# Optimization experiments

Measured on AMD Instinct MI355X. Metric: run time of the kernel, lower is better.

Reference implementation:

```python
import jax, jax.numpy as jnp
import numpy as np

B, T, D, HS = 8, 2048, 768, 64
H = D // HS  # 12 heads
LN_EPS = 1e-5


def setup_inputs() -> dict:
    key = jax.random.key(0)
    ks = jax.random.split(key, 8)
    s = 0.02
    x = jax.random.normal(ks[0], (B, T, D), jnp.float32)
    Wx = jax.random.normal(ks[1], (D, D), jnp.float32) * s
    Ww = jax.random.normal(ks[2], (D, D), jnp.float32) * 0.01  # w_proj.weight ~ N(0,0.01)
    # w_proj bias schedule: logit(1 - linspace(0.9,0.999,H)) per head, expanded over head_size
    r_sched = jnp.linspace(0.9, 0.999, H)
    w_target = 1.0 - r_sched
    bw = jnp.log(w_target / (1.0 - w_target))          # logit
    bw = jnp.repeat(bw[:, None], HS, axis=1).reshape(-1)  # (D,)
    Wk = jax.random.normal(ks[3], (D, D), jnp.float32) * s
    Wv = jax.random.normal(ks[4], (D, D), jnp.float32) * s
    Wr = jax.random.normal(ks[5], (D, D), jnp.float32) * s
    Wo = jax.random.normal(ks[6], (D, D), jnp.float32) * s
    gamma = jnp.ones((D,), jnp.float32)
    beta = jnp.zeros((D,), jnp.float32)
    return {"x": x, "Wx": Wx, "Ww": Ww, "bw": bw, "Wk": Wk, "Wv": Wv,
            "Wr": Wr, "Wo": Wo, "gamma": gamma, "beta": beta}


def _layernorm(x, gamma, beta):
    mu = jnp.mean(x, axis=-1, keepdims=True)
    var = jnp.mean(jnp.square(x - mu), axis=-1, keepdims=True)
    return (x - mu) * jax.lax.rsqrt(var + LN_EPS) * gamma + beta


def _selective_scan(k, v, w):
    """k,v,w: (T,B,H,HS). State S: (B,H,HS,HS).
    S_t = (1 - w_t) * S_{t-1} (decay along key dim) + k_t (x) v_t;  y_t = k_t . S_t."""
    S0 = jnp.zeros((B, H, HS, HS), k.dtype)

    def step(S, inp):
        kt, vt, wt = inp  # each (B,H,HS)
        S = S * (1.0 - wt)[..., :, None] + kt[..., :, None] * vt[..., None, :]
        yt = jnp.einsum('bhi,bhij->bhj', kt, S)
        return S, yt

    _, ys = jax.lax.scan(step, S0, (k, v, w))
    return ys  # (T,B,H,HS)


def reference(x, Wx, Ww, bw, Wk, Wv, Wr, Wo, gamma, beta):
    xn = _layernorm(x, gamma, beta)                       # (B,T,D)
    xp = jnp.einsum('btd,ed->bte', xn, Wx)                # x_proj
    w = jax.nn.sigmoid(jnp.einsum('bte,fe->btf', xp, Ww) + bw)
    k = jnp.einsum('btd,ed->bte', xn, Wk)
    v = jnp.einsum('btd,ed->bte', xn, Wv)
    r = jax.nn.sigmoid(jnp.einsum('btd,ed->bte', xn, Wr))

    def to_scan(a):  # (B,T,D) -> (T,B,H,HS)
        return a.reshape(B, T, H, HS).transpose(1, 0, 2, 3)

    ys = _selective_scan(to_scan(k), to_scan(v), to_scan(w))  # (T,B,H,HS)
    y = ys.transpose(1, 0, 2, 3).reshape(B, T, D)
    y = y * r
    return jnp.einsum('btd,ed->bte', y, Wo)
```

## Files before the change

### kernel.cpp

```cpp
#include <hip/hip_runtime.h>

#define B_ 8
#define T_ 2048
#define D_ 768
#define H_ 12
#define HS_ 64
#define LN_EPS 1e-5f
#define NC 32
#define TC 64

typedef __attribute__((ext_vector_type(8))) short bf16x8;
typedef __attribute__((ext_vector_type(4))) float f32x4;

__device__ __forceinline__ ushort f2bf(float f) {
  unsigned u = __builtin_bit_cast(unsigned, f);
  unsigned r = (u + 0x7FFFu + ((u >> 16) & 1u)) >> 16;
  return (ushort)r;
}
__device__ __forceinline__ float bf2f(ushort u) {
  return __builtin_bit_cast(float, ((unsigned)u) << 16);
}

__device__ __forceinline__ int fragaddr(int t, int i) {
  return ((t >> 4) * 2 + (i >> 5)) * 512 + ((((i >> 3) & 3) * 16) + (t & 15)) * 8 + (i & 7);
}
__device__ __forceinline__ int fragswz(int i) {
  return (((i >> 3) & 3) << 3) ^ (((i >> 5) & 1) << 5);
}

__global__ __launch_bounds__(256) void zero_out_kernel(float* __restrict__ out, int n) {
  for (int i = blockIdx.x * 256 + threadIdx.x; i < n; i += gridDim.x * 256)
    out[i] = 0.f;
}

__global__ __launch_bounds__(256) void prepln_kernel(
    const float* __restrict__ x, const float* __restrict__ gamma,
    const float* __restrict__ beta, ushort* __restrict__ xn,
    const float* __restrict__ w0, const float* __restrict__ w1,
    const float* __restrict__ w2, const float* __restrict__ w3,
    const float* __restrict__ w4, const float* __restrict__ Wx,
    ushort* __restrict__ dst, ushort* __restrict__ WxT) {
  __shared__ ushort tile[32][33];
  const int bid = blockIdx.x;
  if (bid < 4096) {
    const int wv = threadIdx.x >> 6;
    const int lane = threadIdx.x & 63;
    const int row = bid * 4 + wv;
    const float* xr = x + (size_t)row * D_;
    float4 a[3];
#pragma unroll
    for (int s = 0; s < 3; ++s)
      a[s] = *reinterpret_cast<const float4*>(xr + s * 256 + lane * 4);
    float sum = 0.f;
#pragma unroll
    for (int s = 0; s < 3; ++s) sum += a[s].x + a[s].y + a[s].z + a[s].w;
#pragma unroll
    for (int off = 32; off; off >>= 1) sum += __shfl_xor(sum, off);
    float mu = sum * (1.f / 768.f);
    float vs = 0.f;
#pragma unroll
    for (int s = 0; s < 3; ++s) {
      float dx = a[s].x - mu, dy = a[s].y - mu, dz = a[s].z - mu, dw = a[s].w - mu;
      vs += dx * dx + dy * dy + dz * dz + dw * dw;
    }
#pragma unroll
    for (int off = 32; off; off >>= 1) vs += __shfl_xor(vs, off);
    float rs = rsqrtf(vs * (1.f / 768.f) + LN_EPS);
    ushort* orow = xn + (size_t)row * D_;
#pragma unroll
    for (int s = 0; s < 3; ++s) {
      int col = s * 256 + lane * 4;
      float4 g = *reinterpret_cast<const float4*>(gamma + col);
      float4 bb = *reinterpret_cast<const float4*>(beta + col);
      ushort4 o;
      o.x = f2bf((a[s].x - mu) * rs * g.x + bb.x);
      o.y = f2bf((a[s].y - mu) * rs * g.y + bb.y);
      o.z = f2bf((a[s].z - mu) * rs * g.z + bb.z);
      o.w = f2bf((a[s].w - mu) * rs * g.w + bb.w);
      *reinterpret_cast<ushort4*>(orow + col) = o;
    }
  } else if (bid < 4672) {
    const float* srcs[5] = {w0, w1, w2, w3, w4};
    const int slots[5] = {0, 1, 2, 4, 5};
    int idx = ((bid - 4096) * 256 + threadIdx.x) * 4;
#pragma unroll
    for (int s = 0; s < 5; ++s) {
      float4 v = *reinterpret_cast<const float4*>(srcs[s] + idx);
      ushort4 o;
      o.x = f2bf(v.x); o.y = f2bf(v.y); o.z = f2bf(v.z); o.w = f2bf(v.w);
      *reinterpret_cast<ushort4*>(dst + (size_t)slots[s] * 589824 + idx) = o;
    }
  } else {
    const int q = bid - 4672;
    const int bx = (q % 24) * 32;
    const int by = (q / 24) * 32;
    const int tx = threadIdx.x & 31, ty = threadIdx.x >> 5;
#pragma unroll
    for (int r = 0; r < 32; r += 8)
      tile[ty + r][tx] = f2bf(Wx[(size_t)(by + ty + r) * 768 + bx + tx]);
    __syncthreads();
#pragma unroll
    for (int r = 0; r < 32; r += 8)
      WxT[(size_t)(bx + ty + r) * 768 + by + tx] = tile[tx][ty + r];
  }
}

__global__ __launch_bounds__(512, 4) void gemm_p(
    const ushort* __restrict__ A, const ushort* __restrict__ W,
    float* __restrict__ Cf,
    ushort* __restrict__ d0, ushort* __restrict__ d1,
    ushort* __restrict__ d2, ushort* __restrict__ d3, int mode) {
  __shared__ __align__(16) ushort lds[36864];
  const int tid = threadIdx.x;
  const int wid = tid >> 6;
  const int lane = tid & 63;
  const int wr = wid >> 2, wc = wid & 3;
  const int fr = lane & 15, fq = lane >> 4;
  const int m0 = blockIdx.x * 128, n0 = blockIdx.y * 256;
  const int strow = tid >> 2;
  const int stseg = (tid & 3) ^ ((strow >> 1) & 3);
  const int rseg = fq ^ ((fr >> 1) & 3);

  f32x4 acc[4][4];
#pragma unroll
  for (int m = 0; m < 4; ++m)
#pragma unroll
    for (int n = 0; n < 4; ++n) acc[m][n] = (f32x4){0.f, 0.f, 0.f, 0.f};

#define STAGE_T(kk0, b)                                                           \
  {                                                                               \
    const ushort* sa_ = A + (size_t)(m0 + strow) * 768 + (kk0) + stseg * 8;       \
    __builtin_amdgcn_global_load_lds(                                             \
        (const __attribute__((address_space(1))) void*)sa_,                       \
        (__attribute__((address_space(3))) void*)(lds + (b) * 4096 + tid * 8),    \
        16, 0, 0);                                                                \
    _Pragma("unroll") for (int j = 0; j < 2; ++j) {                               \
      const ushort* sb_ =                                                         \
          W + (size_t)(n0 + j * 128 + strow) * 768 + (kk0) + stseg * 8;           \
      __builtin_amdgcn_global_load_lds(                                           \
          (const __attribute__((address_space(1))) void*)sb_,                     \
          (__attribute__((address_space(3))) void*)(lds + 12288 + (b) * 8192 +    \
                                                    j * 4096 + tid * 8),          \
          16, 0, 0);                                                              \
    }                                                                             \
  }

  STAGE_T(0, 0);
  STAGE_T(32, 1);
  STAGE_T(64, 2);
  asm volatile("s_waitcnt vmcnt(6)" ::: "memory");
  __builtin_amdgcn_s_barrier();

#pragma unroll 3
  for (int t = 0; t < 24; ++t) {
    const int buf = t % 3;
    bf16x8 aF[4], bF[4];
#pragma unroll
    for (int mi = 0; mi < 4; ++mi)
      aF[mi] = *reinterpret_cast<const bf16x8*>(
          lds + buf * 4096 + (wr * 64 + mi * 16 + fr) * 32 + rseg * 8);
#pragma unroll
    for (int nf = 0; nf < 4; ++nf)
      bF[nf] = *reinterpret_cast<const bf16x8*>(
          lds + 12288 + buf * 8192 + (wc * 64 + nf * 16 + fr) * 32 + rseg * 8);
    __builtin_amdgcn_s_setprio(1);
#pragma unroll
    for (int mi = 0; mi < 4; ++mi)
#pragma unroll
      for (int nf = 0; nf < 4; ++nf)
        acc[mi][nf] = __builtin_amdgcn_mfma_f32_16x16x32_bf16(
            aF[mi], bF[nf], acc[mi][nf], 0, 0, 0);
    __builtin_amdgcn_s_setprio(0);
    __builtin_amdgcn_s_barrier();
    if (t + 3 < 24) {
      STAGE_T((t + 3) * 32, buf);
      asm volatile("s_waitcnt vmcnt(6)" ::: "memory");
    } else if (t == 21) {
      asm volatile("s_waitcnt vmcnt(3)" ::: "memory");
    } else if (t == 22) {
      asm volatile("s_waitcnt vmcnt(0)" ::: "memory");
    }
    __builtin_amdgcn_s_barrier();
  }
#undef STAGE_T

  const int r0 = fq * 4;
  if (mode == 5) {
    const int sel = n0 >= 2304 ? 3 : n0 >= 1536 ? 2 : n0 >= 768 ? 1 : 0;
    const int nb = n0 - sel * 768;
    if (sel == 1) {
#pragma unroll
      for (int mf = 0; mf < 4; ++mf)
#pragma unroll
        for (int nf = 0; nf < 4; ++nf) {
          int gr = m0 + wr * 64 + mf * 16 + r0;
          int gc = nb + wc * 64 + nf * 16 + fr;
          int b = gr >> 11, t = gr & 2047;
          int c = t >> 6, s0 = t & 63;
          int h = gc >> 6, j = gc & 63;
          size_t addr = ((size_t)((b * 12 + h) * 32 + c)) * 4096 +
                        (size_t)(((j >> 4) * 2 + (s0 >> 5)) * 512 +
                                 (((s0 >> 3) & 3) * 16 + (j & 15)) * 8 + (s0 & 7));
          ushort4 o;
          o.x = f2bf(acc[mf][nf][0]); o.y = f2bf(acc[mf][nf][1]);
          o.z = f2bf(acc[mf][nf][2]); o.w = f2bf(acc[mf][nf][3]);
          *reinterpret_cast<ushort4*>(d1 + addr) = o;
        }
    } else if (sel == 2) {
#pragma unroll
      for (int mf = 0; mf < 4; ++mf)
#pragma unroll
        for (int nf = 0; nf < 4; ++nf) {
          int gr = m0 + wr * 64 + mf * 16 + r0;
          int gc = nb + wc * 64 + nf * 16 + fr;
          int b = gr >> 11, t = gr & 2047;
          int c = t >> 6, tin = t & 63;
          int h = gc >> 6, j = gc & 63;
          size_t addr = ((size_t)((b * 12 + h) * 32 + c)) * 4096 +
                        (size_t)(((tin >> 4) * 64 + ((tin >> 2) & 3) * 16 + (j & 15)) * 16 +
                                 (j >> 4) * 4);
          ushort4 o;
          o.x = f2bf(1.f / (1.f + __expf(-acc[mf][nf][0])));
          o.y = f2bf(1.f / (1.f + __expf(-acc[mf][nf][1])));
          o.z = f2bf(1.f / (1.f + __expf(-acc[mf][nf][2])));
          o.w = f2bf(1.f / (1.f + __expf(-acc[mf][nf][3])));
          *reinterpret_cast<ushort4*>(d2 + addr) = o;
        }
    } else {
      ushort* dst = sel == 0 ? d0 : d3;
#pragma unroll
      for (int mf = 0; mf < 4; ++mf)
#pragma unroll
        for (int nf = 0; nf < 4; ++nf) {
          int gr = m0 + wr * 64 + mf * 16 + r0;
          int gc = nb + wc * 64 + nf * 16 + fr;
#pragma unroll
          for (int rr = 0; rr < 4; ++rr)
            dst[(size_t)(gr + rr) * 768 + gc] = f2bf(acc[mf][nf][rr]);
        }
    }
  } else {
#pragma unroll
    for (int mf = 0; mf < 4; ++mf)
#pragma unroll
      for (int nf = 0; nf < 4; ++nf) {
        int gr = m0 + wr * 64 + mf * 16 + r0;
        int gc = n0 + wc * 64 + nf * 16 + fr;
#pragma unroll
        for (int rr = 0; rr < 4; ++rr)
          Cf[(size_t)(gr + rr) * 768 + gc] = acc[mf][nf][rr];
      }
  }
}

__global__ __launch_bounds__(256) void scan_mc3(
    const ushort* __restrict__ kb, const ushort* __restrict__ zb,
    const ushort* __restrict__ vbF, const float* __restrict__ bwp,
    ushort* __restrict__ McT, float* __restrict__ aend) {
  __shared__ ushort kt[64 * 72];
  __shared__ ushort zt[64 * 72];
  __shared__ ushort kIAfA[4096];
  __shared__ float part[256];
  const int bh = blockIdx.x, c = blockIdx.y;
  const int b = bh / H_, h = bh % H_;
  const int tid = threadIdx.x;
  const int w = tid >> 6, lane = tid & 63;
  const int fr = lane & 15, fq = lane >> 4;
  const int row = tid >> 2, c16 = (tid & 3) * 16;
  const float bwh = bwp[h * 64];

  {
    const ushort* gk = kb + ((size_t)(b * T_ + c * TC + row)) * 768 + h * 64 + c16;
    const ushort* gz = zb + ((size_t)(b * T_ + c * TC + row)) * 768 + h * 64 + c16;
    uint4 k0 = *(const uint4*)gk, k1 = *(const uint4*)(gk + 8);
    uint4 z0 = *(const uint4*)gz, z1 = *(const uint4*)(gz + 8);
    *reinterpret_cast<uint4*>(&kt[row * 72 + c16]) = k0;
    *reinterpret_cast<uint4*>(&kt[row * 72 + c16 + 8]) = k1;
    *reinterpret_cast<uint4*>(&zt[row * 72 + c16]) = z0;
    *reinterpret_cast<uint4*>(&zt[row * 72 + c16 + 8]) = z1;
  }
  bf16x8 vfr[8];
  {
    const ushort* vch = vbF + ((size_t)bh * NC + c) * 4096;
#pragma unroll
    for (int f = 0; f < 8; ++f)
      vfr[f] = *reinterpret_cast<const bf16x8*>(vch + f * 512 + lane * 8);
  }
  __syncthreads();
  float dreg[16];
  float p = 1.f;
#pragma unroll
  for (int tt = 0; tt < 16; ++tt) {
    float z = bf2f(zt[(w * 16 + tt) * 72 + lane]);
    float d = 1.f / (1.f + __expf(z + bwh));
    dreg[tt] = d;
    p *= d;
  }
  part[w * 64 + lane] = p;
  __syncthreads();
  float a = 1.f;
  for (int w2 = 0; w2 < w; ++w2) a *= part[w2 * 64 + lane];
  if (w == 0)
    aend[((size_t)bh * NC + c) * 64 + lane] =
        part[lane] * part[64 + lane] * part[128 + lane] * part[192 + lane];
#pragma unroll
  for (int tt = 0; tt < 16; ++tt) {
    int t = w * 16 + tt;
    float k = bf2f(kt[t * 72 + lane]);
    a *= dreg[tt];
    kIAfA[fragaddr(lane, t)] = f2bf(k / a);
  }
  __syncthreads();

  bf16x8 af2[2];
#pragma unroll
  for (int kk = 0; kk < 2; ++kk)
    af2[kk] = *reinterpret_cast<const bf16x8*>(&kIAfA[(w * 2 + kk) * 512 + lane * 8]);
  f32x4 accM[4];
#pragma unroll
  for (int nf = 0; nf < 4; ++nf) accM[nf] = (f32x4){0.f, 0.f, 0.f, 0.f};
#pragma unroll
  for (int kk = 0; kk < 2; ++kk)
#pragma unroll
    for (int nf = 0; nf < 4; ++nf)
      accM[nf] = __builtin_amdgcn_mfma_f32_16x16x32_bf16(af2[kk], vfr[nf * 2 + kk], accM[nf], 0, 0, 0);
  ushort* mch = McT + ((size_t)bh * NC + c) * 4096;
#pragma unroll
  for (int nf = 0; nf < 4; ++nf) {
    ushort4 o;
    o.x = f2bf(accM[nf][0]); o.y = f2bf(accM[nf][1]);
    o.z = f2bf(accM[nf][2]); o.w = f2bf(accM[nf][3]);
    *reinterpret_cast<ushort4*>(&mch[(nf * 16 + fr) * 64 + w * 16 + fq * 4]) = o;
  }
}

__global__ __launch_bounds__(256) void scan_chain3(
    const ushort* __restrict__ McT, const float* __restrict__ aend,
    ushort* __restrict__ S0F) {
  const int bh = blockIdx.x;
  const int j = threadIdx.x >> 2;
  const int i0 = blockIdx.y * 32 + (threadIdx.x & 3) * 8;
  const int fbase = ((j >> 4) * 2 + (i0 >> 5)) * 512 + (((i0 >> 3) & 3) * 16 + (j & 15)) * 8;
  const ushort* mbase = McT + ((size_t)bh * NC) * 4096 + j * 64 + i0;
  const float* abase = aend + ((size_t)bh * NC) * 64 + i0;
  float S[8];
#pragma unroll
  for (int p = 0; p < 8; ++p) S[p] = 0.f;

  ushort4 m0 = *reinterpret_cast<const ushort4*>(mbase);
  ushort4 m1 = *reinterpret_cast<const ushort4*>(mbase + 4);
  float4 a0 = *(const float4*)(abase);
  float4 a1 = *(const float4*)(abase + 4);
  ushort4 n0 = *reinterpret_cast<const ushort4*>(mbase + 4096);
  ushort4 n1 = *reinterpret_cast<const ushort4*>(mbase + 4096 + 4);
  float4 b0 = *(const float4*)(abase + 64);
  float4 b1 = *(const float4*)(abase + 64 + 4);

  for (int c = 0; c < NC; ++c) {
    int cn2 = c + 2 < NC ? c + 2 : NC - 1;
    ushort4 p0 = *reinterpret_cast<const ushort4*>(mbase + (size_t)cn2 * 4096);
    ushort4 p1 = *reinterpret_cast<const ushort4*>(mbase + (size_t)cn2 * 4096 + 4);
    float4 q0 = *(const float4*)(abase + (size_t)cn2 * 64);
    float4 q1 = *(const float4*)(abase + (size_t)cn2 * 64 + 4);

    ushort* s0 = S0F + ((size_t)bh * NC + c) * 4096 + fbase;
    ushort4 o0, o1;
    o0.x = f2bf(S[0]); o0.y = f2bf(S[1]); o0.z = f2bf(S[2]); o0.w = f2bf(S[3]);
    o1.x = f2bf(S[4]); o1.y = f2bf(S[5]); o1.z = f2bf(S[6]); o1.w = f2bf(S[7]);
    *reinterpret_cast<ushort4*>(s0) = o0;
    *reinterpret_cast<ushort4*>(s0 + 4) = o1;

    S[0] = a0.x * (S[0] + bf2f(m0.x));
    S[1] = a0.y * (S[1] + bf2f(m0.y));
    S[2] = a0.z * (S[2] + bf2f(m0.z));
    S[3] = a0.w * (S[3] + bf2f(m0.w));
    S[4] = a1.x * (S[4] + bf2f(m1.x));
    S[5] = a1.y * (S[5] + bf2f(m1.y));
    S[6] = a1.z * (S[6] + bf2f(m1.z));
    S[7] = a1.w * (S[7] + bf2f(m1.w));

    m0 = n0; m1 = n1; a0 = b0; a1 = b1;
    n0 = p0; n1 = p1; b0 = q0; b1 = q1;
  }
}

__global__ __launch_bounds__(256, 2) void scan_y3(
    const ushort* __restrict__ kb, const ushort* __restrict__ zb,
    const ushort* __restrict__ vbF, const ushort* __restrict__ rbF,
    const ushort* __restrict__ S0F, const float* __restrict__ bwp,
    ushort* __restrict__ yrow) {
  __shared__ ushort kt[64 * 72];
  __shared__ ushort zt[64 * 72];
  __shared__ ushort kAf[4096];
  __shared__ ushort kIAfB[4096];
  __shared__ ushort Am[64 * 72];
  __shared__ float part[256];
  const int bh = blockIdx.x, c = blockIdx.y;
  const int b = bh / H_, h = bh % H_;
  const int tid = threadIdx.x;
  const int w = tid >> 6, lane = tid & 63;
  const int fr = lane & 15, fq = lane >> 4;
  const int row = tid >> 2, c16 = (tid & 3) * 16;
  const float bwh = bwp[h * 64];
  const int swz = fragswz(lane);

  {
    const ushort* gk = kb + ((size_t)(b * T_ + c * TC + row)) * 768 + h * 64 + c16;
    const ushort* gz = zb + ((size_t)(b * T_ + c * TC + row)) * 768 + h * 64 + c16;
    uint4 k0 = *(const uint4*)gk, k1 = *(const uint4*)(gk + 8);
    uint4 z0 = *(const uint4*)gz, z1 = *(const uint4*)(gz + 8);
    *reinterpret_cast<uint4*>(&kt[row * 72 + c16]) = k0;
    *reinterpret_cast<uint4*>(&kt[row * 72 + c16 + 8]) = k1;
    *reinterpret_cast<uint4*>(&zt[row * 72 + c16]) = z0;
    *reinterpret_cast<uint4*>(&zt[row * 72 + c16 + 8]) = z1;
  }
  bf16x8 vfr[8], s0fr[8];
  {
    const ushort* vch = vbF + ((size_t)bh * NC + c) * 4096;
    const ushort* s0ch = S0F + ((size_t)bh * NC + c) * 4096;
#pragma unroll
    for (int f = 0; f < 8; ++f) {
      vfr[f] = *reinterpret_cast<const bf16x8*>(vch + f * 512 + lane * 8);
      s0fr[f] = *reinterpret_cast<const bf16x8*>(s0ch + f * 512 + lane * 8);
    }
  }
  ushort4 rp0, rp1, rp2, rp3;
  {
    const ushort* rch = rbF + ((size_t)bh * NC + c) * 4096 + tid * 16;
    rp0 = *reinterpret_cast<const ushort4*>(rch);
    rp1 = *reinterpret_cast<const ushort4*>(rch + 4);
    rp2 = *reinterpret_cast<const ushort4*>(rch + 8);
    rp3 = *reinterpret_cast<const ushort4*>(rch + 12);
  }
  const ushort rl[16] = {rp0.x, rp0.y, rp0.z, rp0.w, rp1.x, rp1.y, rp1.z, rp1.w,
                         rp2.x, rp2.y, rp2.z, rp2.w, rp3.x, rp3.y, rp3.z, rp3.w};
  __syncthreads();
  float dreg[16];
  float p = 1.f;
#pragma unroll
  for (int tt = 0; tt < 16; ++tt) {
    float z = bf2f(zt[(w * 16 + tt) * 72 + lane]);
    float d = 1.f / (1.f + __expf(z + bwh));
    dreg[tt] = d;
    p *= d;
  }
  part[w * 64 + lane] = p;
  __syncthreads();
  float a = 1.f;
  for (int w2 = 0; w2 < w; ++w2) a *= part[w2 * 64 + lane];
#pragma unroll
  for (int tt = 0; tt < 16; ++tt) {
    int t = w * 16 + tt;
    float k = bf2f(kt[t * 72 + lane]);
    a *= dreg[tt];
    int ad = fragaddr(t, lane) ^ swz;
    kAf[ad] = f2bf(k * a);
    kIAfB[ad] = f2bf(k / a);
  }
  __syncthreads();

  bf16x8 af[2];
#pragma unroll
  for (int kk = 0; kk < 2; ++kk) {
    int ra = ((w * 2 + kk) * 512 + lane * 8) ^ (((lane >> 4) << 3) ^ (kk << 5));
    af[kk] = *reinterpret_cast<const bf16x8*>(&kAf[ra]);
  }
  {
    f32x4 accA[4];
#pragma unroll
    for (int nf = 0; nf < 4; ++nf) accA[nf] = (f32x4){0.f, 0.f, 0.f, 0.f};
#pragma unroll
    for (int kk = 0; kk < 2; ++kk)
#pragma unroll
      for (int nf = 0; nf < 4; ++nf) {
        int rb8 = ((nf * 2 + kk) * 512 + lane * 8) ^ (((lane >> 4) << 3) ^ (kk << 5));
        bf16x8 b8 = *reinterpret_cast<const bf16x8*>(&kIAfB[rb8]);
        accA[nf] = __builtin_amdgcn_mfma_f32_16x16x32_bf16(af[kk], b8, accA[nf], 0, 0, 0);
      }
#pragma unroll
    for (int nf = 0; nf < 4; ++nf)
#pragma unroll
      for (int q = 0; q < 4; ++q) {
        int t = w * 16 + fq * 4 + q;
        int s = nf * 16 + fr;
        Am[t * 72 + s] = f2bf((s <= t) ? accA[nf][q] : 0.f);
      }
  }
  __syncthreads();

  f32x4 accY[4];
#pragma unroll
  for (int nf = 0; nf < 4; ++nf) accY[nf] = (f32x4){0.f, 0.f, 0.f, 0.f};
#pragma unroll
  for (int kk = 0; kk < 2; ++kk)
#pragma unroll
    for (int nf = 0; nf < 4; ++nf)
      accY[nf] = __builtin_amdgcn_mfma_f32_16x16x32_bf16(af[kk], s0fr[nf * 2 + kk], accY[nf], 0, 0, 0);
#pragma unroll
  for (int kk = 0; kk < 2; ++kk) {
    bf16x8 am8 = *reinterpret_cast<const bf16x8*>(&Am[(w * 16 + fr) * 72 + kk * 32 + fq * 8]);
#pragma unroll
    for (int nf = 0; nf < 4; ++nf)
      accY[nf] = __builtin_amdgcn_mfma_f32_16x16x32_bf16(am8, vfr[nf * 2 + kk], accY[nf], 0, 0, 0);
  }
#pragma unroll
  for (int nf = 0; nf < 4; ++nf)
#pragma unroll
    for (int q = 0; q < 4; ++q) {
      int t = w * 16 + fq * 4 + q;
      int j = nf * 16 + fr;
      size_t go = ((size_t)(b * T_ + c * TC + t)) * 768 + h * 64 + j;
      yrow[go] = f2bf(accY[nf][q] * bf2f(rl[nf * 4 + q]));
    }
}

extern "C" void kernel_launch(void* const* d_in, const int* in_sizes, int n_in,
                              void* d_out, int out_size, void* d_ws, size_t ws_size,
                              hipStream_t stream) {
  const float* x     = (const float*)d_in[0];
  const float* Wx    = (const float*)d_in[1];
  const float* Ww    = (const float*)d_in[2];
  const float* bw    = (const float*)d_in[3];
  const float* Wk    = (const float*)d_in[4];
  const float* Wv    = (const float*)d_in[5];
  const float* Wr    = (const float*)d_in[6];
  const float* Wo    = (const float*)d_in[7];
  const float* gamma = (const float*)d_in[8];
  const float* beta  = (const float*)d_in[9];
  float* out = (float*)d_out;

  const size_t NEED = 208404480ull;
  if (ws_size < NEED) {
    zero_out_kernel<<<2048, 256, 0, stream>>>(out, out_size);
    return;
  }

  char* ws = (char*)d_ws;
  ushort* xn  = (ushort*)ws;
  ushort* wb  = (ushort*)(ws + 25165824);
  ushort* WxT = (ushort*)(ws + 32243712);
  ushort* kb  = (ushort*)(ws + 57409536);
  ushort* vbF = (ushort*)(ws + 82575360);
  ushort* rbF = (ushort*)(ws + 107741184);
  ushort* yr  = (ushort*)(ws + 132907008);
  ushort* zb  = (ushort*)(ws + 158072832);
  ushort* McT = (ushort*)ws;
  ushort* S0F = (ushort*)(ws + 32243712);
  float*  aendb = (float*)(ws + 132907008);

  ushort* WcatB = wb;
  ushort* Mb  = wb + 3 * 589824;
  ushort* WoB = wb + 4 * 589824;
  ushort* WwB = wb + 5 * 589824;

  prepln_kernel<<<5248, 256, 0, stream>>>(x, gamma, beta, xn,
                                          Wk, Wv, Wr, Wo, Ww, Wx, wb, WxT);
  gemm_p<<<dim3(6, 3), 512, 0, stream>>>(WwB, WxT, nullptr, Mb, nullptr, nullptr,
                                         nullptr, 5);
  gemm_p<<<dim3(128, 12), 512, 0, stream>>>(xn, WcatB, nullptr, kb, vbF, rbF, zb, 5);

  scan_mc3<<<dim3(96, NC), 256, 0, stream>>>(kb, zb, vbF, bw, McT, aendb);
  scan_chain3<<<dim3(96, 2), 256, 0, stream>>>(McT, aendb, S0F);
  scan_y3<<<dim3(96, NC), 256, 0, stream>>>(kb, zb, vbF, rbF, S0F, bw, yr);

  gemm_p<<<dim3(128, 3), 512, 0, stream>>>(yr, WoB, out, nullptr, nullptr, nullptr,
                                           nullptr, 0);
}
```

Before: 223.7 us.

## Enlarge GEMM block tile to 256x256 with 4 waves each computing 128x128

The GEMM kernel moves from 128x256 tiles with 8 waves (64x64 per wave) to 256x256 tiles with 4 waves (128x128 per wave). Each wave now holds an 8x8 grid of MFMA accumulators, which raises arithmetic intensity per LDS fragment load and halves the A-operand traffic per output. The cost is 256 accumulator floats per thread, launch bounds of 1 block per CU, and far fewer blocks: 768 for the main GEMM, 192 for the output GEMM and 9 for the small weight GEMM. Occupancy and latency hiding drop, and the smaller grids may not fill all CUs.

```diff
diff --git a/kernel.cpp b/kernel.cpp
--- a/kernel.cpp
+++ b/kernel.cpp
@@ -105,42 +105,49 @@
   }
 }
 
-__global__ __launch_bounds__(512, 4) void gemm_p(
+__global__ __launch_bounds__(256, 1) void gemm_w(
     const ushort* __restrict__ A, const ushort* __restrict__ W,
     float* __restrict__ Cf,
     ushort* __restrict__ d0, ushort* __restrict__ d1,
     ushort* __restrict__ d2, ushort* __restrict__ d3, int mode) {
-  __shared__ __align__(16) ushort lds[36864];
+  __shared__ __align__(16) ushort lds[49152];
   const int tid = threadIdx.x;
   const int wid = tid >> 6;
   const int lane = tid & 63;
-  const int wr = wid >> 2, wc = wid & 3;
+  const int wr = wid >> 1, wc = wid & 1;
   const int fr = lane & 15, fq = lane >> 4;
-  const int m0 = blockIdx.x * 128, n0 = blockIdx.y * 256;
-  const int strow = tid >> 2;
-  const int stseg = (tid & 3) ^ ((strow >> 1) & 3);
+  const int m0 = blockIdx.x * 256, n0 = blockIdx.y * 256;
   const int rseg = fq ^ ((fr >> 1) & 3);
 
-  f32x4 acc[4][4];
-#pragma unroll
-  for (int m = 0; m < 4; ++m)
-#pragma unroll
-    for (int n = 0; n < 4; ++n) acc[m][n] = (f32x4){0.f, 0.f, 0.f, 0.f};
+  size_t offA[4], offB[4];
+#pragma unroll
+  for (int l = 0; l < 4; ++l) {
+    int g = l * 256 + tid;
+    int row = g >> 2;
+    int seg = (g & 3) ^ ((row >> 1) & 3);
+    offA[l] = (size_t)(m0 + row) * 768 + seg * 8;
+    offB[l] = (size_t)(n0 + row) * 768 + seg * 8;
+  }
+
+  f32x4 acc[8][8];
+#pragma unroll
+  for (int m = 0; m < 8; ++m)
+#pragma unroll
+    for (int n = 0; n < 8; ++n) acc[m][n] = (f32x4){0.f, 0.f, 0.f, 0.f};
 
 #define STAGE_T(kk0, b)                                                           \
   {                                                                               \
-    const ushort* sa_ = A + (size_t)(m0 + strow) * 768 + (kk0) + stseg * 8;       \
-    __builtin_amdgcn_global_load_lds(                                             \
-        (const __attribute__((address_space(1))) void*)sa_,                       \
-        (__attribute__((address_space(3))) void*)(lds + (b) * 4096 + tid * 8),    \
-        16, 0, 0);                                                                \
-    _Pragma("unroll") for (int j = 0; j < 2; ++j) {                               \
-      const ushort* sb_ =                                                         \
-          W + (size_t)(n0 + j * 128 + strow) * 768 + (kk0) + stseg * 8;           \
+    _Pragma("unroll") for (int l = 0; l < 4; ++l) {                               \
       __builtin_amdgcn_global_load_lds(                                           \
-          (const __attribute__((address_space(1))) void*)sb_,                     \
-          (__attribute__((address_space(3))) void*)(lds + 12288 + (b) * 8192 +    \
-                                                    j * 4096 + tid * 8),          \
+          (const __attribute__((address_space(1))) void*)(A + offA[l] + (kk0)),   \
+          (__attribute__((address_space(3))) void*)(lds + (b) * 8192 + l * 2048 + tid * 8), \
+          16, 0, 0);                                                              \
+    }                                                                             \
+    _Pragma("unroll") for (int l = 0; l < 4; ++l) {                               \
+      __builtin_amdgcn_global_load_lds(                                           \
+          (const __attribute__((address_space(1))) void*)(W + offB[l] + (kk0)),   \
+          (__attribute__((address_space(3))) void*)(lds + 24576 + (b) * 8192 +    \
+                                                    l * 2048 + tid * 8),          \
           16, 0, 0);                                                              \
     }                                                                             \
   }
@@ -148,35 +155,34 @@
   STAGE_T(0, 0);
   STAGE_T(32, 1);
   STAGE_T(64, 2);
-  asm volatile("s_waitcnt vmcnt(6)" ::: "memory");
+  asm volatile("s_waitcnt vmcnt(16)" ::: "memory");
   __builtin_amdgcn_s_barrier();
 
 #pragma unroll 3
   for (int t = 0; t < 24; ++t) {
     const int buf = t % 3;
-    bf16x8 aF[4], bF[4];
-#pragma unroll
-    for (int mi = 0; mi < 4; ++mi)
-      aF[mi] = *reinterpret_cast<const bf16x8*>(
-          lds + buf * 4096 + (wr * 64 + mi * 16 + fr) * 32 + rseg * 8);
-#pragma unroll
-    for (int nf = 0; nf < 4; ++nf)
+    bf16x8 bF[8];
+#pragma unroll
+    for (int nf = 0; nf < 8; ++nf)
       bF[nf] = *reinterpret_cast<const bf16x8*>(
-          lds + 12288 + buf * 8192 + (wc * 64 + nf * 16 + fr) * 32 + rseg * 8);
+          lds + 24576 + buf * 8192 + (wc * 128 + nf * 16 + fr) * 32 + rseg * 8);
     __builtin_amdgcn_s_setprio(1);
 #pragma unroll
-    for (int mi = 0; mi < 4; ++mi)
-#pragma unroll
-      for (int nf = 0; nf < 4; ++nf)
+    for (int mi = 0; mi < 8; ++mi) {
+      bf16x8 aF = *reinterpret_cast<const bf16x8*>(
+          lds + buf * 8192 + (wr * 128 + mi * 16 + fr) * 32 + rseg * 8);
+#pragma unroll
+      for (int nf = 0; nf < 8; ++nf)
         acc[mi][nf] = __builtin_amdgcn_mfma_f32_16x16x32_bf16(
-            aF[mi], bF[nf], acc[mi][nf], 0, 0, 0);
+            aF, bF[nf], acc[mi][nf], 0, 0, 0);
+    }
     __builtin_amdgcn_s_setprio(0);
     __builtin_amdgcn_s_barrier();
     if (t + 3 < 24) {
       STAGE_T((t + 3) * 32, buf);
-      asm volatile("s_waitcnt vmcnt(6)" ::: "memory");
+      asm volatile("s_waitcnt vmcnt(16)" ::: "memory");
     } else if (t == 21) {
-      asm volatile("s_waitcnt vmcnt(3)" ::: "memory");
+      asm volatile("s_waitcnt vmcnt(8)" ::: "memory");
     } else if (t == 22) {
       asm volatile("s_waitcnt vmcnt(0)" ::: "memory");
     }
@@ -190,11 +196,11 @@
     const int nb = n0 - sel * 768;
     if (sel == 1) {
 #pragma unroll
-      for (int mf = 0; mf < 4; ++mf)
-#pragma unroll
-        for (int nf = 0; nf < 4; ++nf) {
-          int gr = m0 + wr * 64 + mf * 16 + r0;
-          int gc = nb + wc * 64 + nf * 16 + fr;
+      for (int mf = 0; mf < 8; ++mf)
+#pragma unroll
+        for (int nf = 0; nf < 8; ++nf) {
+          int gr = m0 + wr * 128 + mf * 16 + r0;
+          int gc = nb + wc * 128 + nf * 16 + fr;
           int b = gr >> 11, t = gr & 2047;
           int c = t >> 6, s0 = t & 63;
           int h = gc >> 6, j = gc & 63;
@@ -208,11 +214,11 @@
         }
     } else if (sel == 2) {
 #pragma unroll
-      for (int mf = 0; mf < 4; ++mf)
-#pragma unroll
-        for (int nf = 0; nf < 4; ++nf) {
-          int gr = m0 + wr * 64 + mf * 16 + r0;
-          int gc = nb + wc * 64 + nf * 16 + fr;
+      for (int mf = 0; mf < 8; ++mf)
+#pragma unroll
+        for (int nf = 0; nf < 8; ++nf) {
+          int gr = m0 + wr * 128 + mf * 16 + r0;
+          int gc = nb + wc * 128 + nf * 16 + fr;
           int b = gr >> 11, t = gr & 2047;
           int c = t >> 6, tin = t & 63;
           int h = gc >> 6, j = gc & 63;
@@ -229,11 +235,11 @@
     } else {
       ushort* dst = sel == 0 ? d0 : d3;
 #pragma unroll
-      for (int mf = 0; mf < 4; ++mf)
-#pragma unroll
-        for (int nf = 0; nf < 4; ++nf) {
-          int gr = m0 + wr * 64 + mf * 16 + r0;
-          int gc = nb + wc * 64 + nf * 16 + fr;
+      for (int mf = 0; mf < 8; ++mf)
+#pragma unroll
+        for (int nf = 0; nf < 8; ++nf) {
+          int gr = m0 + wr * 128 + mf * 16 + r0;
+          int gc = nb + wc * 128 + nf * 16 + fr;
 #pragma unroll
           for (int rr = 0; rr < 4; ++rr)
             dst[(size_t)(gr + rr) * 768 + gc] = f2bf(acc[mf][nf][rr]);
@@ -241,11 +247,11 @@
     }
   } else {
 #pragma unroll
-    for (int mf = 0; mf < 4; ++mf)
-#pragma unroll
-      for (int nf = 0; nf < 4; ++nf) {
-        int gr = m0 + wr * 64 + mf * 16 + r0;
-        int gc = n0 + wc * 64 + nf * 16 + fr;
+    for (int mf = 0; mf < 8; ++mf)
+#pragma unroll
+      for (int nf = 0; nf < 8; ++nf) {
+        int gr = m0 + wr * 128 + mf * 16 + r0;
+        int gc = n0 + wc * 128 + nf * 16 + fr;
 #pragma unroll
         for (int rr = 0; rr < 4; ++rr)
           Cf[(size_t)(gr + rr) * 768 + gc] = acc[mf][nf][rr];
@@ -555,14 +561,14 @@
 
   prepln_kernel<<<5248, 256, 0, stream>>>(x, gamma, beta, xn,
                                           Wk, Wv, Wr, Wo, Ww, Wx, wb, WxT);
-  gemm_p<<<dim3(6, 3), 512, 0, stream>>>(WwB, WxT, nullptr, Mb, nullptr, nullptr,
+  gemm_w<<<dim3(3, 3), 256, 0, stream>>>(WwB, WxT, nullptr, Mb, nullptr, nullptr,
                                          nullptr, 5);
-  gemm_p<<<dim3(128, 12), 512, 0, stream>>>(xn, WcatB, nullptr, kb, vbF, rbF, zb, 5);
+  gemm_w<<<dim3(64, 12), 256, 0, stream>>>(xn, WcatB, nullptr, kb, vbF, rbF, zb, 5);
 
   scan_mc3<<<dim3(96, NC), 256, 0, stream>>>(kb, zb, vbF, bw, McT, aendb);
   scan_chain3<<<dim3(96, 2), 256, 0, stream>>>(McT, aendb, S0F);
   scan_y3<<<dim3(96, NC), 256, 0, stream>>>(kb, zb, vbF, rbF, S0F, bw, yr);
 
-  gemm_p<<<dim3(128, 3), 512, 0, stream>>>(yr, WoB, out, nullptr, nullptr, nullptr,
-                                           nullptr, 0);
-}
+  gemm_w<<<dim3(64, 3), 256, 0, stream>>>(yr, WoB, out, nullptr, nullptr, nullptr,
+                                          nullptr, 0);
+}
```

New measurement: 496.7 us. +122.1%, slower.
